# Performance work log

Measured on AMD Instinct MI355X. Metric: run time of the kernel, lower is better.

The kernel has to match this reference:

```python
import jax, jax.numpy as jnp
import numpy as np

HEADS = 8
NUM_LANDMARKS = 256
PINV_ITERS = 6
KERNEL = 33
PAD = KERNEL // 2


def moore_penrose_iter_pinv(x, iters=PINV_ITERS):
    abs_x = jnp.abs(x)
    col = abs_x.sum(axis=-1)
    row = abs_x.sum(axis=-2)
    z = jnp.swapaxes(x, -1, -2) / (jnp.max(col) * jnp.max(row))
    I = jnp.eye(x.shape[-1], dtype=x.dtype)
    for _ in range(iters):
        xz = x @ z
        z = 0.25 * z @ (13.0 * I - xz @ (15.0 * I - xz @ (7.0 * I - xz)))
    return z


def setup_inputs() -> dict:
    key = jax.random.key(0)
    k1, k2, k3, k4 = jax.random.split(key, 4)
    b, h, n, d = 2, HEADS, 8192, 64
    q = jax.random.normal(k1, (b, h, n, d), dtype=jnp.float32)
    k = jax.random.normal(k2, (b, h, n, d), dtype=jnp.float32)
    v = jax.random.normal(k3, (b, h, n, d), dtype=jnp.float32)
    conv_w = jax.random.normal(k4, (HEADS, 1, KERNEL, 1), dtype=jnp.float32) * 0.05
    return {"q": q, "k": k, "v": v, "conv_w": conv_w}


def reference(q, k, v, conv_w):
    b, h, n, d = q.shape
    m = NUM_LANDMARKS
    l = n // m  # n chosen divisible by m, so no padding branch

    # landmarks: mean over contiguous groups of size l
    q_land = q.reshape(b, h, m, l, d).sum(axis=-2) / l  # [b,h,m,d]
    k_land = k.reshape(b, h, m, l, d).sum(axis=-2) / l

    sim1 = jnp.einsum('bhid,bhjd->bhij', q, k_land)       # [b,h,n,m]
    sim2 = jnp.einsum('bhid,bhjd->bhij', q_land, k_land)  # [b,h,m,m]
    sim3 = jnp.einsum('bhid,bhjd->bhij', q_land, k)       # [b,h,m,n]

    attn1 = jax.nn.softmax(sim1, axis=-1)
    attn2 = jax.nn.softmax(sim2, axis=-1)
    attn3 = jax.nn.softmax(sim3, axis=-1)

    attn2_inv = moore_penrose_iter_pinv(attn2, PINV_ITERS)

    out = attn1 @ (attn2_inv @ (attn3 @ v))  # [b,h,n,d]

    # depthwise residual conv over sequence dim (Conv2d(h,h,(33,1),groups=h,bias=False) on v)
    res = jax.lax.conv_general_dilated(
        v, conv_w,
        window_strides=(1, 1),
        padding=((PAD, PAD), (0, 0)),
        dimension_numbers=('NCHW', 'OIHW', 'NCHW'),
        feature_group_count=HEADS,
    )
    return out + res
```

## Files before the change

kernel.cpp:

```cpp
#include <hip/hip_runtime.h>


#define N_SEQ 8192
#define NBH   16
#define MLAND 256
#define DHEAD 64
#define NSPLIT3 8

#define QT_STRIDE 132
#define KP_OFF    8448
#define WC_OFF    12800
#define FL_SMEM   17152

typedef __attribute__((ext_vector_type(8))) short bfrag;
typedef __attribute__((ext_vector_type(4))) float f32x4;

__device__ __forceinline__ void fma8(float (&o)[8], float p, const float4& a, const float4& b) {
    o[0] += p * a.x; o[1] += p * a.y; o[2] += p * a.z; o[3] += p * a.w;
    o[4] += p * b.x; o[5] += p * b.y; o[6] += p * b.z; o[7] += p * b.w;
}

__device__ __forceinline__ unsigned short f2bf(float f) {
    unsigned u = __float_as_uint(f);
    unsigned r = u + 0x7fffu + ((u >> 16) & 1u);
    return (unsigned short)(r >> 16);
}
__device__ __forceinline__ float bf2f(unsigned short h) {
    return __uint_as_float(((unsigned)h) << 16);
}

__device__ __forceinline__ void splitbf(float v, unsigned short& h, unsigned short& l) {
    unsigned bits = __float_as_uint(v);
    h = (unsigned short)(bits >> 16);
    float r = v - __uint_as_float(bits & 0xffff0000u);
    l = (unsigned short)(__float_as_uint(r) >> 16);
}

__device__ __forceinline__ void stage16(const float* __restrict__ src,
                                        unsigned short* dh, unsigned short* dl) {
    unsigned* ph = (unsigned*)dh;
    unsigned* pl = (unsigned*)dl;
    #pragma unroll
    for (int o = 0; o < 16; o += 4) {
        float4 a = *(const float4*)(src + o);
        float vv[4] = {a.x, a.y, a.z, a.w};
        unsigned short h[4], l[4];
        #pragma unroll
        for (int u = 0; u < 4; ++u) splitbf(vv[u], h[u], l[u]);
        ph[o / 2]     = (unsigned)h[0] | ((unsigned)h[1] << 16);
        ph[o / 2 + 1] = (unsigned)h[2] | ((unsigned)h[3] << 16);
        pl[o / 2]     = (unsigned)l[0] | ((unsigned)l[1] << 16);
        pl[o / 2 + 1] = (unsigned)l[2] | ((unsigned)l[3] << 16);
    }
}

__global__ __launch_bounds__(64) void k_landmarks(
    const float* __restrict__ q, const float* __restrict__ k,
    float* __restrict__ ql, float* __restrict__ kl)
{
    int mi = blockIdx.x & 255;
    int bh = blockIdx.x >> 8;
    const float* src = blockIdx.y ? k : q;
    float*       dst = blockIdx.y ? kl : ql;
    int t = threadIdx.x;
    const float* s = src + ((size_t)bh * N_SEQ + (size_t)mi * 32) * DHEAD;
    float acc = 0.f;
    #pragma unroll
    for (int j = 0; j < 32; ++j) acc += s[j * DHEAD + t];
    dst[((size_t)bh * MLAND + mi) * DHEAD + t] = acc * (1.f / 32.f);
}

__global__ __launch_bounds__(256) void k_sim2_softmax(
    const float* __restrict__ ql, const float* __restrict__ kl,
    float* __restrict__ attn2)
{
    int bh = blockIdx.x >> 8;
    int i  = blockIdx.x & 255;
    int t  = threadIdx.x;
    __shared__ float qrow[DHEAD];
    __shared__ float wred[8];
    if (t < DHEAD) qrow[t] = ql[((size_t)bh * MLAND + i) * DHEAD + t];
    __syncthreads();
    const float* krow = kl + ((size_t)bh * MLAND + t) * DHEAD;
    float s = 0.f;
    #pragma unroll
    for (int kk = 0; kk < DHEAD; kk += 4) {
        float4 k4 = *(const float4*)(krow + kk);
        s += qrow[kk] * k4.x + qrow[kk + 1] * k4.y + qrow[kk + 2] * k4.z + qrow[kk + 3] * k4.w;
    }
    float m = s;
    #pragma unroll
    for (int o = 32; o > 0; o >>= 1) m = fmaxf(m, __shfl_xor(m, o, 64));
    int wave = t >> 6, lane = t & 63;
    if (lane == 0) wred[wave] = m;
    __syncthreads();
    float bm = fmaxf(fmaxf(wred[0], wred[1]), fmaxf(wred[2], wred[3]));
    float e = __expf(s - bm);
    float sum = e;
    #pragma unroll
    for (int o = 32; o > 0; o >>= 1) sum += __shfl_xor(sum, o, 64);
    if (lane == 0) wred[4 + wave] = sum;
    __syncthreads();
    float bs = wred[4] + wred[5] + wred[6] + wred[7];
    attn2[((size_t)bh * MLAND + i) * MLAND + t] = e / bs;
}

__global__ __launch_bounds__(256) void k_scale_reduce(
    const float* __restrict__ x, float* __restrict__ scl)
{
    int bh = blockIdx.x, t = threadIdx.x;
    const float* xb = x + (size_t)bh * MLAND * MLAND;
    float colsum = 0.f, rowsum = 0.f;
    for (int i = 0; i < MLAND; ++i) colsum += xb[(size_t)i * MLAND + t];
    for (int j = 0; j < MLAND; ++j) rowsum += xb[(size_t)t * MLAND + j];
    __shared__ float red[256];
    red[t] = rowsum;
    __syncthreads();
    for (int o = 128; o > 0; o >>= 1) {
        if (t < o) red[t] = fmaxf(red[t], red[t + o]);
        __syncthreads();
    }
    if (t == 0) atomicMax((unsigned int*)&scl[0], __float_as_uint(red[0]));
    __syncthreads();
    red[t] = colsum;
    __syncthreads();
    for (int o = 128; o > 0; o >>= 1) {
        if (t < o) red[t] = fmaxf(red[t], red[t + o]);
        __syncthreads();
    }
    if (t == 0) atomicMax((unsigned int*)&scl[1], __float_as_uint(red[0]));
}

__global__ __launch_bounds__(256) void k_zinit(
    const float* __restrict__ x, float* __restrict__ z,
    const float* __restrict__ scl)
{
    __shared__ float tile[32][33];
    int bh = blockIdx.z;
    int i0 = blockIdx.y * 32, j0 = blockIdx.x * 32;
    int t = threadIdx.x;
    int lx = t & 31, ly = t >> 5;
    const float* xb = x + (size_t)bh * MLAND * MLAND;
    float*       zb = z + (size_t)bh * MLAND * MLAND;
    #pragma unroll
    for (int p = 0; p < 4; ++p)
        tile[ly + 8 * p][lx] = xb[(size_t)(i0 + ly + 8 * p) * MLAND + j0 + lx];
    __syncthreads();
    float inv = 1.0f / (scl[0] * scl[1]);
    #pragma unroll
    for (int p = 0; p < 4; ++p)
        zb[(size_t)(j0 + ly + 8 * p) * MLAND + i0 + lx] = tile[lx][ly + 8 * p] * inv;
}

__global__ __launch_bounds__(256) void k_bmm_mfma(
    const float* __restrict__ A, const float* __restrict__ B, float* __restrict__ C,
    int N, float diag, float bscale, float outscale)
{
    __shared__ unsigned short sm[4 * 64 * 72];
    unsigned short* Ah = sm;
    unsigned short* Al = sm + 64 * 72;
    unsigned short* Bh = sm + 2 * 64 * 72;
    unsigned short* Bl = sm + 3 * 64 * 72;

    int bh = blockIdx.z;
    const float* Ab = A + (size_t)bh * 65536;
    const float* Bb = B + (size_t)bh * 256 * N;
    float*       Cb = C + (size_t)bh * 256 * N;
    int m0 = blockIdx.y * 64, n0 = blockIdx.x * 64;
    int t = threadIdx.x;
    int wave = t >> 6, lane = t & 63;
    int l15 = lane & 15, quad = lane >> 4;

    f32x4 acc[4] = {};

    for (int kc = 0; kc < 256; kc += 64) {
        __syncthreads();
        {
            int m = t & 63, ks = (t >> 6) * 16;
            const float* src = Ab + (size_t)(m0 + m) * 256 + kc + ks;
            unsigned short h[16], l[16];
            #pragma unroll
            for (int o = 0; o < 16; o += 4) {
                float4 a = *(const float4*)(src + o);
                float vv[4] = {a.x, a.y, a.z, a.w};
                #pragma unroll
                for (int u = 0; u < 4; ++u) {
                    h[o + u] = f2bf(vv[u]);
                    l[o + u] = f2bf(vv[u] - bf2f(h[o + u]));
                }
            }
            unsigned* dh = (unsigned*)&Ah[m * 72 + ks];
            unsigned* dl = (unsigned*)&Al[m * 72 + ks];
            #pragma unroll
            for (int o = 0; o < 8; ++o) {
                dh[o] = (unsigned)h[2 * o] | ((unsigned)h[2 * o + 1] << 16);
                dl[o] = (unsigned)l[2 * o] | ((unsigned)l[2 * o + 1] << 16);
            }
        }
        {
            int kk = t & 63, ns = (t >> 6) * 16;
            int gk = kc + kk;
            const float* src = Bb + (size_t)gk * N + n0 + ns;
            #pragma unroll
            for (int o = 0; o < 16; o += 4) {
                float4 bv = *(const float4*)(src + o);
                float vv[4] = {bv.x, bv.y, bv.z, bv.w};
                #pragma unroll
                for (int u = 0; u < 4; ++u) {
                    float val = bscale * vv[u];
                    if (gk == n0 + ns + o + u) val += diag;
                    unsigned short hh = f2bf(val);
                    Bh[(ns + o + u) * 72 + kk] = hh;
                    Bl[(ns + o + u) * 72 + kk] = f2bf(val - bf2f(hh));
                }
            }
        }
        __syncthreads();

        #pragma unroll
        for (int k0 = 0; k0 < 64; k0 += 32) {
            int kf = k0 + quad * 8;
            int am = wave * 16 + l15;
            bfrag ah = *(const bfrag*)&Ah[am * 72 + kf];
            bfrag al = *(const bfrag*)&Al[am * 72 + kf];
            #pragma unroll
            for (int j = 0; j < 4; ++j) {
                int bn = j * 16 + l15;
                bfrag bhf = *(const bfrag*)&Bh[bn * 72 + kf];
                bfrag blf = *(const bfrag*)&Bl[bn * 72 + kf];
                acc[j] = __builtin_amdgcn_mfma_f32_16x16x32_bf16(al, bhf, acc[j], 0, 0, 0);
                acc[j] = __builtin_amdgcn_mfma_f32_16x16x32_bf16(ah, blf, acc[j], 0, 0, 0);
                acc[j] = __builtin_amdgcn_mfma_f32_16x16x32_bf16(ah, bhf, acc[j], 0, 0, 0);
            }
        }
    }

    #pragma unroll
    for (int j = 0; j < 4; ++j) {
        #pragma unroll
        for (int r = 0; r < 4; ++r) {
            int row = m0 + wave * 16 + quad * 4 + r;
            Cb[(size_t)row * N + n0 + j * 16 + l15] = acc[j][r] * outscale;
        }
    }
}

__global__ __launch_bounds__(256, 2) void k_attn3_partial(
    const float* __restrict__ ql, const float* __restrict__ k,
    const float* __restrict__ v, float* __restrict__ pO,
    float* __restrict__ pm, float* __restrict__ pl)
{
    __shared__ __align__(16) unsigned short sm3[36864];
    unsigned short* QH = sm3;
    unsigned short* QL = sm3 + 4608;
    unsigned short* KH = sm3 + 9216;
    unsigned short* KL = sm3 + 13824;
    unsigned short* VH = sm3 + 18432;
    unsigned short* VL = sm3 + 23040;
    unsigned short* PH = sm3 + 27648;
    unsigned short* PL = sm3 + 32256;

    int sp = blockIdx.x;
    int m0 = blockIdx.y * 64;
    int bh = blockIdx.z;
    int t = threadIdx.x;
    int wave = t >> 6, lane = t & 63;
    int l15 = lane & 15, quad = lane >> 4;

    {
        int row = t & 63, ds = (t >> 6) * 16;
        const float* src = ql + ((size_t)bh * MLAND + m0 + row) * DHEAD + ds;
        stage16(src, &QH[row * 72 + ds], &QL[row * 72 + ds]);
    }
    __syncthreads();

    bfrag aqh[2], aql[2];
    #pragma unroll
    for (int ks = 0; ks < 2; ++ks) {
        aqh[ks] = *(const bfrag*)&QH[(wave * 16 + l15) * 72 + ks * 32 + quad * 8];
        aql[ks] = *(const bfrag*)&QL[(wave * 16 + l15) * 72 + ks * 32 + quad * 8];
    }

    f32x4 O[4] = {};
    float M[4], L[4];
    #pragma unroll
    for (int r = 0; r < 4; ++r) { M[r] = -1e30f; L[r] = 0.f; }

    const float* kb = k + (size_t)bh * N_SEQ * DHEAD;
    const float* vb = v + (size_t)bh * N_SEQ * DHEAD;

    for (int cc = 0; cc < 16; ++cc) {
        int c0 = sp * 1024 + cc * 64;
        __syncthreads();
        {
            int key = t & 63, ds = (t >> 6) * 16;
            stage16(kb + (size_t)(c0 + key) * DHEAD + ds,
                    &KH[key * 72 + ds], &KL[key * 72 + ds]);
        }
        {
            int key = t & 63, dq = (t >> 6) * 16;
            const float* src = vb + (size_t)(c0 + key) * DHEAD + dq;
            #pragma unroll
            for (int o = 0; o < 16; o += 4) {
                float4 a = *(const float4*)(src + o);
                float vv[4] = {a.x, a.y, a.z, a.w};
                #pragma unroll
                for (int u = 0; u < 4; ++u) {
                    unsigned short h, l;
                    splitbf(vv[u], h, l);
                    VH[(dq + o + u) * 72 + key] = h;
                    VL[(dq + o + u) * 72 + key] = l;
                }
            }
        }
        __syncthreads();

        f32x4 S4[4] = {};
        __builtin_amdgcn_s_setprio(1);
        #pragma unroll
        for (int ks = 0; ks < 2; ++ks) {
            #pragma unroll
            for (int ni = 0; ni < 4; ++ni) {
                bfrag bkh = *(const bfrag*)&KH[(ni * 16 + l15) * 72 + ks * 32 + quad * 8];
                bfrag bkl = *(const bfrag*)&KL[(ni * 16 + l15) * 72 + ks * 32 + quad * 8];
                S4[ni] = __builtin_amdgcn_mfma_f32_16x16x32_bf16(aql[ks], bkh, S4[ni], 0, 0, 0);
                S4[ni] = __builtin_amdgcn_mfma_f32_16x16x32_bf16(aqh[ks], bkl, S4[ni], 0, 0, 0);
                S4[ni] = __builtin_amdgcn_mfma_f32_16x16x32_bf16(aqh[ks], bkh, S4[ni], 0, 0, 0);
            }
        }
        __builtin_amdgcn_s_setprio(0);

        #pragma unroll
        for (int r = 0; r < 4; ++r) {
            float mv = fmaxf(fmaxf(S4[0][r], S4[1][r]), fmaxf(S4[2][r], S4[3][r]));
            mv = fmaxf(mv, __shfl_xor(mv, 1, 16));
            mv = fmaxf(mv, __shfl_xor(mv, 2, 16));
            mv = fmaxf(mv, __shfl_xor(mv, 4, 16));
            mv = fmaxf(mv, __shfl_xor(mv, 8, 16));
            float nM = fmaxf(M[r], mv);
            float alpha = __expf(M[r] - nM);
            M[r] = nM;
            float rs = 0.f;
            #pragma unroll
            for (int ni = 0; ni < 4; ++ni) {
                float p = __expf(S4[ni][r] - nM);
                S4[ni][r] = p;
                rs += p;
            }
            rs += __shfl_xor(rs, 1, 16);
            rs += __shfl_xor(rs, 2, 16);
            rs += __shfl_xor(rs, 4, 16);
            rs += __shfl_xor(rs, 8, 16);
            L[r] = L[r] * alpha + rs;
            #pragma unroll
            for (int ni = 0; ni < 4; ++ni) O[ni][r] *= alpha;
        }

        #pragma unroll
        for (int ni = 0; ni < 4; ++ni) {
            #pragma unroll
            for (int r = 0; r < 4; ++r) {
                int row = wave * 16 + quad * 4 + r;
                int col = ni * 16 + l15;
                unsigned short h, l;
                splitbf(S4[ni][r], h, l);
                PH[row * 72 + col] = h;
                PL[row * 72 + col] = l;
            }
        }

        __builtin_amdgcn_s_setprio(1);
        #pragma unroll
        for (int ks = 0; ks < 2; ++ks) {
            bfrag aph = *(const bfrag*)&PH[(wave * 16 + l15) * 72 + ks * 32 + quad * 8];
            bfrag apl = *(const bfrag*)&PL[(wave * 16 + l15) * 72 + ks * 32 + quad * 8];
            #pragma unroll
            for (int ni = 0; ni < 4; ++ni) {
                bfrag bvh = *(const bfrag*)&VH[(ni * 16 + l15) * 72 + ks * 32 + quad * 8];
                bfrag bvl = *(const bfrag*)&VL[(ni * 16 + l15) * 72 + ks * 32 + quad * 8];
                O[ni] = __builtin_amdgcn_mfma_f32_16x16x32_bf16(apl, bvh, O[ni], 0, 0, 0);
                O[ni] = __builtin_amdgcn_mfma_f32_16x16x32_bf16(aph, bvl, O[ni], 0, 0, 0);
                O[ni] = __builtin_amdgcn_mfma_f32_16x16x32_bf16(aph, bvh, O[ni], 0, 0, 0);
            }
        }
        __builtin_amdgcn_s_setprio(0);
    }

    int base = (bh * NSPLIT3 + sp) * MLAND + m0;
    #pragma unroll
    for (int r = 0; r < 4; ++r) {
        int row = wave * 16 + quad * 4 + r;
        if (l15 == 0) { pm[base + row] = M[r]; pl[base + row] = L[r]; }
        #pragma unroll
        for (int ni = 0; ni < 4; ++ni)
            pO[(size_t)(base + row) * DHEAD + ni * 16 + l15] = O[ni][r];
    }
}

__global__ __launch_bounds__(64) void k_attn3_combine(
    const float* __restrict__ pO, const float* __restrict__ pm,
    const float* __restrict__ pl, float* __restrict__ kv)
{
    int bh = blockIdx.x >> 8;
    int m  = blockIdx.x & 255;
    int d  = threadIdx.x;
    float M = -1e30f;
    #pragma unroll
    for (int s = 0; s < NSPLIT3; ++s) M = fmaxf(M, pm[(bh * NSPLIT3 + s) * MLAND + m]);
    float L = 0.f, O = 0.f;
    #pragma unroll
    for (int s = 0; s < NSPLIT3; ++s) {
        int base = (bh * NSPLIT3 + s) * MLAND + m;
        float w = __expf(pm[base] - M);
        L += pl[base] * w;
        O += w * pO[(size_t)base * DHEAD + d];
    }
    kv[((size_t)bh * MLAND + m) * DHEAD + d] = O / L;
}

__global__ __launch_bounds__(256, 2) void k_attn1_out(
    const float* __restrict__ q, const float* __restrict__ kl,
    const float* __restrict__ W, const float* __restrict__ v,
    const float* __restrict__ cw, float* __restrict__ out)
{
    __shared__ __align__(16) float smem[FL_SMEM];
    __shared__ float wgt[33];
    int bh = blockIdx.y;
    int r0 = blockIdx.x * 128;
    int t = threadIdx.x;
    int wave = t >> 6, lane = t & 63;
    int ly = lane >> 3, lx = lane & 7;
    int rb = wave * 32 + ly * 4;

    if (t < 33) wgt[t] = cw[(bh & 7) * 33 + t];
    {
        int m = t >> 1, k0 = (t & 1) * 32;
        const float* src = q + ((size_t)bh * N_SEQ + r0 + m) * DHEAD + k0;
        #pragma unroll
        for (int kk = 0; kk < 32; kk += 4) {
            float4 a = *(const float4*)(src + kk);
            smem[(k0 + kk + 0) * QT_STRIDE + m] = a.x;
            smem[(k0 + kk + 1) * QT_STRIDE + m] = a.y;
            smem[(k0 + kk + 2) * QT_STRIDE + m] = a.z;
            smem[(k0 + kk + 3) * QT_STRIDE + m] = a.w;
        }
    }

    float S[4][8], O[4][8] = {};
    float M[4], L[4];
    #pragma unroll
    for (int i = 0; i < 4; ++i) { M[i] = -1e30f; L[i] = 0.f; }

    for (int mc = 0; mc < 4; ++mc) {
        __syncthreads();
        {
            int j = t & 63, kq = t >> 6;
            const float* src = kl + ((size_t)bh * MLAND + mc * 64 + j) * DHEAD + kq * 16;
            #pragma unroll
            for (int o = 0; o < 16; o += 4) {
                float4 a = *(const float4*)(src + o);
                smem[KP_OFF + (kq * 16 + o + 0) * 68 + j] = a.x;
                smem[KP_OFF + (kq * 16 + o + 1) * 68 + j] = a.y;
                smem[KP_OFF + (kq * 16 + o + 2) * 68 + j] = a.z;
                smem[KP_OFF + (kq * 16 + o + 3) * 68 + j] = a.w;
            }
        }
        {
            int j = t & 63, dq = t >> 6;
            const float* src = W + ((size_t)bh * MLAND + mc * 64 + j) * DHEAD + dq * 16;
            #pragma unroll
            for (int o = 0; o < 16; o += 4)
                *(float4*)&smem[WC_OFF + j * 68 + dq * 16 + o] = *(const float4*)(src + o);
        }
        __syncthreads();

        #pragma unroll
        for (int i = 0; i < 4; ++i)
            #pragma unroll
            for (int j = 0; j < 8; ++j) S[i][j] = 0.f;
        #pragma unroll 4
        for (int kk = 0; kk < DHEAD; ++kk) {
            float4 a4 = *(const float4*)&smem[kk * QT_STRIDE + rb];
            float4 b0 = *(const float4*)&smem[KP_OFF + kk * 68 + lx * 8];
            float4 b1 = *(const float4*)&smem[KP_OFF + kk * 68 + lx * 8 + 4];
            float av[4] = {a4.x, a4.y, a4.z, a4.w};
            #pragma unroll
            for (int i = 0; i < 4; ++i) fma8(S[i], av[i], b0, b1);
        }

        #pragma unroll
        for (int i = 0; i < 4; ++i) {
            float mv = S[i][0];
            #pragma unroll
            for (int j = 1; j < 8; ++j) mv = fmaxf(mv, S[i][j]);
            mv = fmaxf(mv, __shfl_xor(mv, 4, 8));
            mv = fmaxf(mv, __shfl_xor(mv, 2, 8));
            mv = fmaxf(mv, __shfl_xor(mv, 1, 8));
            float nM = fmaxf(M[i], mv);
            float alpha = __expf(M[i] - nM);
            M[i] = nM;
            float rs = 0.f;
            #pragma unroll
            for (int j = 0; j < 8; ++j) { S[i][j] = __expf(S[i][j] - nM); rs += S[i][j]; }
            rs += __shfl_xor(rs, 4, 8);
            rs += __shfl_xor(rs, 2, 8);
            rs += __shfl_xor(rs, 1, 8);
            L[i] = L[i] * alpha + rs;
            #pragma unroll
            for (int j = 0; j < 8; ++j) O[i][j] *= alpha;
        }

        #pragma unroll 2
        for (int lsrc = 0; lsrc < 8; ++lsrc) {
            #pragma unroll
            for (int jq = 0; jq < 8; ++jq) {
                int j = lsrc * 8 + jq;
                float4 v0 = *(const float4*)&smem[WC_OFF + j * 68 + lx * 8];
                float4 v1 = *(const float4*)&smem[WC_OFF + j * 68 + lx * 8 + 4];
                #pragma unroll
                for (int i = 0; i < 4; ++i) {
                    float p = __shfl(S[i][jq], lsrc, 8);
                    fma8(O[i], p, v0, v1);
                }
            }
        }
    }

    float inv[4];
    #pragma unroll
    for (int i = 0; i < 4; ++i) inv[i] = 1.0f / L[i];

    __syncthreads();
    for (int rr = t; rr < 160; rr += 256) {
        int gr = r0 - 16 + rr;
        bool ok = (gr >= 0) && (gr < N_SEQ);
        const float* src = v + ((size_t)bh * N_SEQ + gr) * DHEAD;
        #pragma unroll
        for (int c = 0; c < 64; c += 4) {
            float4 val = ok ? *(const float4*)(src + c) : make_float4(0.f, 0.f, 0.f, 0.f);
            *(float4*)&smem[rr * 68 + c] = val;
        }
    }
    __syncthreads();

    float res[4][8] = {};
    #pragma unroll
    for (int w = 0; w < 36; ++w) {
        float4 va = *(const float4*)&smem[(rb + w) * 68 + lx * 8];
        float4 vb4 = *(const float4*)&smem[(rb + w) * 68 + lx * 8 + 4];
        #pragma unroll
        for (int i = 0; i < 4; ++i) {
            if (w - i >= 0 && w - i <= 32) {
                float wv = wgt[w - i];
                fma8(res[i], wv, va, vb4);
            }
        }
    }

    #pragma unroll
    for (int i = 0; i < 4; ++i) {
        float* dst = out + ((size_t)bh * N_SEQ + r0 + rb + i) * DHEAD + lx * 8;
        *(float4*)dst = make_float4(O[i][0] * inv[i] + res[i][0], O[i][1] * inv[i] + res[i][1],
                                    O[i][2] * inv[i] + res[i][2], O[i][3] * inv[i] + res[i][3]);
        *(float4*)(dst + 4) = make_float4(O[i][4] * inv[i] + res[i][4], O[i][5] * inv[i] + res[i][5],
                                          O[i][6] * inv[i] + res[i][6], O[i][7] * inv[i] + res[i][7]);
    }
}

extern "C" void kernel_launch(void* const* d_in, const int* in_sizes, int n_in,
                              void* d_out, int out_size, void* d_ws, size_t ws_size,
                              hipStream_t stream)
{
    (void)in_sizes; (void)n_in; (void)out_size; (void)ws_size;
    const float* q  = (const float*)d_in[0];
    const float* k  = (const float*)d_in[1];
    const float* v  = (const float*)d_in[2];
    const float* cw = (const float*)d_in[3];
    float* out = (float*)d_out;
    float* ws  = (float*)d_ws;

    const size_t LM = (size_t)NBH * MLAND * DHEAD;
    const size_t MM = (size_t)NBH * MLAND * MLAND;
    float* ql  = ws;
    float* kl  = ql  + LM;
    float* x   = kl  + LM;
    float* z   = x   + MM;
    float* z2  = z   + MM;
    float* xz  = z2  + MM;
    float* t2  = xz  + MM;
    float* t3  = t2  + MM;
    float* kv  = t3  + MM;
    float* W   = kv  + LM;
    float* scl = W   + LM;
    float* pm  = scl + 16;
    float* pl  = pm + (size_t)NBH * 16 * MLAND;

    float* pO = z2;

    hipMemsetAsync(scl, 0, 32, stream);

    k_landmarks<<<dim3(NBH * MLAND, 2), 64, 0, stream>>>(q, k, ql, kl);
    k_sim2_softmax<<<NBH * MLAND, 256, 0, stream>>>(ql, kl, x);
    k_scale_reduce<<<NBH, 256, 0, stream>>>(x, scl);
    k_zinit<<<dim3(8, 8, NBH), 256, 0, stream>>>(x, z, scl);

    k_attn3_partial<<<dim3(NSPLIT3, 4, NBH), 256, 0, stream>>>(ql, k, v, pO, pm, pl);
    k_attn3_combine<<<NBH * MLAND, 64, 0, stream>>>(pO, pm, pl, kv);

    float* zc = z;
    float* zn = z2;
    for (int it = 0; it < 6; ++it) {
        k_bmm_mfma<<<dim3(4, 4, NBH), 256, 0, stream>>>(x,  zc, xz, 256,  0.f,  1.f, 1.f);
        k_bmm_mfma<<<dim3(4, 4, NBH), 256, 0, stream>>>(xz, xz, t2, 256,  7.f, -1.f, 1.f);
        k_bmm_mfma<<<dim3(4, 4, NBH), 256, 0, stream>>>(xz, t2, t3, 256, 15.f, -1.f, 1.f);
        k_bmm_mfma<<<dim3(4, 4, NBH), 256, 0, stream>>>(zc, t3, zn, 256, 13.f, -1.f, 0.25f);
        float* tt = zc; zc = zn; zn = tt;
    }
    k_bmm_mfma<<<dim3(1, 4, NBH), 256, 0, stream>>>(zc, kv, W, 64, 0.f, 1.f, 1.f);

    k_attn1_out<<<dim3(64, NBH), 256, 0, stream>>>(q, kl, W, v, cw, out);
}
```

Measured before the change: 707.3 us.

## Move attn1 output to split-fp16 MFMA and split conv residual into separate kernel

Replaces the scalar-FMA attn1 softmax and output kernel with one using fp16 MFMA. Each operand is split into high and low fp16 parts and three MFMAs are issued to keep near-fp32 accuracy, with W pre-scaled by 1/64 to avoid fp16 overflow. The depthwise conv residual moves into a separate kernel that reads the attention output back and adds to it. This trades an extra launch and an extra read/write of the output for much higher matrix throughput and smaller tiles of 64 rows.

```diff
diff --git a/kernel.cpp b/kernel.cpp
--- a/kernel.cpp
+++ b/kernel.cpp
@@ -7,12 +7,8 @@
 #define DHEAD 64
 #define NSPLIT3 8
 
-#define QT_STRIDE 132
-#define KP_OFF    8448
-#define WC_OFF    12800
-#define FL_SMEM   17152
-
 typedef __attribute__((ext_vector_type(8))) short bfrag;
+typedef __attribute__((ext_vector_type(8))) _Float16 hfrag;
 typedef __attribute__((ext_vector_type(4))) float f32x4;
 
 __device__ __forceinline__ void fma8(float (&o)[8], float p, const float4& a, const float4& b) {
@@ -36,6 +32,13 @@
     l = (unsigned short)(__float_as_uint(r) >> 16);
 }
 
+__device__ __forceinline__ void splith(float v, unsigned short& h, unsigned short& l) {
+    _Float16 hf = (_Float16)v;
+    _Float16 lf = (_Float16)(v - (float)hf);
+    h = __builtin_bit_cast(unsigned short, hf);
+    l = __builtin_bit_cast(unsigned short, lf);
+}
+
 __device__ __forceinline__ void stage16(const float* __restrict__ src,
                                         unsigned short* dh, unsigned short* dl) {
     unsigned* ph = (unsigned*)dh;
@@ -47,6 +50,24 @@
         unsigned short h[4], l[4];
         #pragma unroll
         for (int u = 0; u < 4; ++u) splitbf(vv[u], h[u], l[u]);
+        ph[o / 2]     = (unsigned)h[0] | ((unsigned)h[1] << 16);
+        ph[o / 2 + 1] = (unsigned)h[2] | ((unsigned)h[3] << 16);
+        pl[o / 2]     = (unsigned)l[0] | ((unsigned)l[1] << 16);
+        pl[o / 2 + 1] = (unsigned)l[2] | ((unsigned)l[3] << 16);
+    }
+}
+
+__device__ __forceinline__ void stageh16(const float* __restrict__ src,
+                                         unsigned short* dh, unsigned short* dl) {
+    unsigned* ph = (unsigned*)dh;
+    unsigned* pl = (unsigned*)dl;
+    #pragma unroll
+    for (int o = 0; o < 16; o += 4) {
+        float4 a = *(const float4*)(src + o);
+        float vv[4] = {a.x, a.y, a.z, a.w};
+        unsigned short h[4], l[4];
+        #pragma unroll
+        for (int u = 0; u < 4; ++u) splith(vv[u], h[u], l[u]);
         ph[o / 2]     = (unsigned)h[0] | ((unsigned)h[1] << 16);
         ph[o / 2 + 1] = (unsigned)h[2] | ((unsigned)h[3] << 16);
         pl[o / 2]     = (unsigned)l[0] | ((unsigned)l[1] << 16);
@@ -418,12 +439,160 @@
     kv[((size_t)bh * MLAND + m) * DHEAD + d] = O / L;
 }
 
-__global__ __launch_bounds__(256, 2) void k_attn1_out(
+__global__ __launch_bounds__(256, 2) void k_attn1_mfma(
     const float* __restrict__ q, const float* __restrict__ kl,
-    const float* __restrict__ W, const float* __restrict__ v,
-    const float* __restrict__ cw, float* __restrict__ out)
-{
-    __shared__ __align__(16) float smem[FL_SMEM];
+    const float* __restrict__ W, float* __restrict__ out)
+{
+    __shared__ __align__(16) unsigned short sm1[36864];
+    unsigned short* QH = sm1;
+    unsigned short* QL = sm1 + 4608;
+    unsigned short* KH = sm1 + 9216;
+    unsigned short* KL = sm1 + 13824;
+    unsigned short* WH = sm1 + 18432;
+    unsigned short* WL = sm1 + 23040;
+    unsigned short* PH = sm1 + 27648;
+    unsigned short* PL = sm1 + 32256;
+
+    int bh = blockIdx.y;
+    int r0 = blockIdx.x * 64;
+    int t = threadIdx.x;
+    int wave = t >> 6, lane = t & 63;
+    int l15 = lane & 15, quad = lane >> 4;
+
+    {
+        int row = t & 63, ds = (t >> 6) * 16;
+        const float* src = q + ((size_t)bh * N_SEQ + r0 + row) * DHEAD + ds;
+        stageh16(src, &QH[row * 72 + ds], &QL[row * 72 + ds]);
+    }
+    __syncthreads();
+
+    hfrag aqh[2], aql[2];
+    #pragma unroll
+    for (int ks = 0; ks < 2; ++ks) {
+        aqh[ks] = *(const hfrag*)&QH[(wave * 16 + l15) * 72 + ks * 32 + quad * 8];
+        aql[ks] = *(const hfrag*)&QL[(wave * 16 + l15) * 72 + ks * 32 + quad * 8];
+    }
+
+    f32x4 O4[4] = {};
+    float M[4], L[4];
+    #pragma unroll
+    for (int r = 0; r < 4; ++r) { M[r] = -1e30f; L[r] = 0.f; }
+
+    for (int mc = 0; mc < 4; ++mc) {
+        __syncthreads();
+        {
+            int key = t & 63, ds = (t >> 6) * 16;
+            stageh16(kl + ((size_t)bh * MLAND + mc * 64 + key) * DHEAD + ds,
+                     &KH[key * 72 + ds], &KL[key * 72 + ds]);
+        }
+        {
+            int key = t & 63, dq = (t >> 6) * 16;
+            const float* src = W + ((size_t)bh * MLAND + mc * 64 + key) * DHEAD + dq;
+            #pragma unroll
+            for (int o = 0; o < 16; o += 4) {
+                float4 a = *(const float4*)(src + o);
+                float vv[4] = {a.x * 0.015625f, a.y * 0.015625f,
+                               a.z * 0.015625f, a.w * 0.015625f};
+                #pragma unroll
+                for (int u = 0; u < 4; ++u) {
+                    unsigned short h, l;
+                    splith(vv[u], h, l);
+                    WH[(dq + o + u) * 72 + key] = h;
+                    WL[(dq + o + u) * 72 + key] = l;
+                }
+            }
+        }
+        __syncthreads();
+
+        f32x4 S4[4] = {};
+        __builtin_amdgcn_s_setprio(1);
+        #pragma unroll
+        for (int ks = 0; ks < 2; ++ks) {
+            #pragma unroll
+            for (int ni = 0; ni < 4; ++ni) {
+                hfrag bkh = *(const hfrag*)&KH[(ni * 16 + l15) * 72 + ks * 32 + quad * 8];
+                hfrag bkl = *(const hfrag*)&KL[(ni * 16 + l15) * 72 + ks * 32 + quad * 8];
+                S4[ni] = __builtin_amdgcn_mfma_f32_16x16x32_f16(aql[ks], bkh, S4[ni], 0, 0, 0);
+                S4[ni] = __builtin_amdgcn_mfma_f32_16x16x32_f16(aqh[ks], bkl, S4[ni], 0, 0, 0);
+                S4[ni] = __builtin_amdgcn_mfma_f32_16x16x32_f16(aqh[ks], bkh, S4[ni], 0, 0, 0);
+            }
+        }
+        __builtin_amdgcn_s_setprio(0);
+
+        #pragma unroll
+        for (int r = 0; r < 4; ++r) {
+            float mv = fmaxf(fmaxf(S4[0][r], S4[1][r]), fmaxf(S4[2][r], S4[3][r]));
+            mv = fmaxf(mv, __shfl_xor(mv, 1, 16));
+            mv = fmaxf(mv, __shfl_xor(mv, 2, 16));
+            mv = fmaxf(mv, __shfl_xor(mv, 4, 16));
+            mv = fmaxf(mv, __shfl_xor(mv, 8, 16));
+            float nM = fmaxf(M[r], mv);
+            float alpha = __expf(M[r] - nM);
+            M[r] = nM;
+            float rs = 0.f;
+            #pragma unroll
+            for (int ni = 0; ni < 4; ++ni) {
+                float p = __expf(S4[ni][r] - nM);
+                S4[ni][r] = p;
+                rs += p;
+            }
+            rs += __shfl_xor(rs, 1, 16);
+            rs += __shfl_xor(rs, 2, 16);
+            rs += __shfl_xor(rs, 4, 16);
+            rs += __shfl_xor(rs, 8, 16);
+            L[r] = L[r] * alpha + rs;
+            #pragma unroll
+            for (int ni = 0; ni < 4; ++ni) O4[ni][r] *= alpha;
+        }
+
+        #pragma unroll
+        for (int ni = 0; ni < 4; ++ni) {
+            #pragma unroll
+            for (int r = 0; r < 4; ++r) {
+                int row = wave * 16 + quad * 4 + r;
+                int col = ni * 16 + l15;
+                unsigned short h, l;
+                splith(S4[ni][r], h, l);
+                PH[row * 72 + col] = h;
+                PL[row * 72 + col] = l;
+            }
+        }
+
+        __builtin_amdgcn_s_setprio(1);
+        #pragma unroll
+        for (int ks = 0; ks < 2; ++ks) {
+            hfrag aph = *(const hfrag*)&PH[(wave * 16 + l15) * 72 + ks * 32 + quad * 8];
+            hfrag apl = *(const hfrag*)&PL[(wave * 16 + l15) * 72 + ks * 32 + quad * 8];
+            #pragma unroll
+            for (int ni = 0; ni < 4; ++ni) {
+                hfrag bwh = *(const hfrag*)&WH[(ni * 16 + l15) * 72 + ks * 32 + quad * 8];
+                hfrag bwl = *(const hfrag*)&WL[(ni * 16 + l15) * 72 + ks * 32 + quad * 8];
+                O4[ni] = __builtin_amdgcn_mfma_f32_16x16x32_f16(apl, bwh, O4[ni], 0, 0, 0);
+                O4[ni] = __builtin_amdgcn_mfma_f32_16x16x32_f16(aph, bwl, O4[ni], 0, 0, 0);
+                O4[ni] = __builtin_amdgcn_mfma_f32_16x16x32_f16(aph, bwh, O4[ni], 0, 0, 0);
+            }
+        }
+        __builtin_amdgcn_s_setprio(0);
+    }
+
+    float inv[4];
+    #pragma unroll
+    for (int r = 0; r < 4; ++r) inv[r] = 64.0f / L[r];
+    #pragma unroll
+    for (int r = 0; r < 4; ++r) {
+        int row = wave * 16 + quad * 4 + r;
+        float* dst = out + ((size_t)bh * N_SEQ + r0 + row) * DHEAD;
+        #pragma unroll
+        for (int ni = 0; ni < 4; ++ni)
+            dst[ni * 16 + l15] = O4[ni][r] * inv[r];
+    }
+}
+
+__global__ __launch_bounds__(256) void k_conv_add(
+    const float* __restrict__ v, const float* __restrict__ cw,
+    float* __restrict__ out)
+{
+    __shared__ __align__(16) float smem[160 * 68];
     __shared__ float wgt[33];
     int bh = blockIdx.y;
     int r0 = blockIdx.x * 128;
@@ -433,104 +602,7 @@
     int rb = wave * 32 + ly * 4;
 
     if (t < 33) wgt[t] = cw[(bh & 7) * 33 + t];
-    {
-        int m = t >> 1, k0 = (t & 1) * 32;
-        const float* src = q + ((size_t)bh * N_SEQ + r0 + m) * DHEAD + k0;
-        #pragma unroll
-        for (int kk = 0; kk < 32; kk += 4) {
-            float4 a = *(const float4*)(src + kk);
-            smem[(k0 + kk + 0) * QT_STRIDE + m] = a.x;
-            smem[(k0 + kk + 1) * QT_STRIDE + m] = a.y;
-            smem[(k0 + kk + 2) * QT_STRIDE + m] = a.z;
-            smem[(k0 + kk + 3) * QT_STRIDE + m] = a.w;
-        }
-    }
-
-    float S[4][8], O[4][8] = {};
-    float M[4], L[4];
-    #pragma unroll
-    for (int i = 0; i < 4; ++i) { M[i] = -1e30f; L[i] = 0.f; }
-
-    for (int mc = 0; mc < 4; ++mc) {
-        __syncthreads();
-        {
-            int j = t & 63, kq = t >> 6;
-            const float* src = kl + ((size_t)bh * MLAND + mc * 64 + j) * DHEAD + kq * 16;
-            #pragma unroll
-            for (int o = 0; o < 16; o += 4) {
-                float4 a = *(const float4*)(src + o);
-                smem[KP_OFF + (kq * 16 + o + 0) * 68 + j] = a.x;
-                smem[KP_OFF + (kq * 16 + o + 1) * 68 + j] = a.y;
-                smem[KP_OFF + (kq * 16 + o + 2) * 68 + j] = a.z;
-                smem[KP_OFF + (kq * 16 + o + 3) * 68 + j] = a.w;
-            }
-        }
-        {
-            int j = t & 63, dq = t >> 6;
-            const float* src = W + ((size_t)bh * MLAND + mc * 64 + j) * DHEAD + dq * 16;
-            #pragma unroll
-            for (int o = 0; o < 16; o += 4)
-                *(float4*)&smem[WC_OFF + j * 68 + dq * 16 + o] = *(const float4*)(src + o);
-        }
-        __syncthreads();
-
-        #pragma unroll
-        for (int i = 0; i < 4; ++i)
-            #pragma unroll
-            for (int j = 0; j < 8; ++j) S[i][j] = 0.f;
-        #pragma unroll 4
-        for (int kk = 0; kk < DHEAD; ++kk) {
-            float4 a4 = *(const float4*)&smem[kk * QT_STRIDE + rb];
-            float4 b0 = *(const float4*)&smem[KP_OFF + kk * 68 + lx * 8];
-            float4 b1 = *(const float4*)&smem[KP_OFF + kk * 68 + lx * 8 + 4];
-            float av[4] = {a4.x, a4.y, a4.z, a4.w};
-            #pragma unroll
-            for (int i = 0; i < 4; ++i) fma8(S[i], av[i], b0, b1);
-        }
-
-        #pragma unroll
-        for (int i = 0; i < 4; ++i) {
-            float mv = S[i][0];
-            #pragma unroll
-            for (int j = 1; j < 8; ++j) mv = fmaxf(mv, S[i][j]);
-            mv = fmaxf(mv, __shfl_xor(mv, 4, 8));
-            mv = fmaxf(mv, __shfl_xor(mv, 2, 8));
-            mv = fmaxf(mv, __shfl_xor(mv, 1, 8));
-            float nM = fmaxf(M[i], mv);
-            float alpha = __expf(M[i] - nM);
-            M[i] = nM;
-            float rs = 0.f;
-            #pragma unroll
-            for (int j = 0; j < 8; ++j) { S[i][j] = __expf(S[i][j] - nM); rs += S[i][j]; }
-            rs += __shfl_xor(rs, 4, 8);
-            rs += __shfl_xor(rs, 2, 8);
-            rs += __shfl_xor(rs, 1, 8);
-            L[i] = L[i] * alpha + rs;
-            #pragma unroll
-            for (int j = 0; j < 8; ++j) O[i][j] *= alpha;
-        }
-
-        #pragma unroll 2
-        for (int lsrc = 0; lsrc < 8; ++lsrc) {
-            #pragma unroll
-            for (int jq = 0; jq < 8; ++jq) {
-                int j = lsrc * 8 + jq;
-                float4 v0 = *(const float4*)&smem[WC_OFF + j * 68 + lx * 8];
-                float4 v1 = *(const float4*)&smem[WC_OFF + j * 68 + lx * 8 + 4];
-                #pragma unroll
-                for (int i = 0; i < 4; ++i) {
-                    float p = __shfl(S[i][jq], lsrc, 8);
-                    fma8(O[i], p, v0, v1);
-                }
-            }
-        }
-    }
-
-    float inv[4];
-    #pragma unroll
-    for (int i = 0; i < 4; ++i) inv[i] = 1.0f / L[i];
-
-    __syncthreads();
+
     for (int rr = t; rr < 160; rr += 256) {
         int gr = r0 - 16 + rr;
         bool ok = (gr >= 0) && (gr < N_SEQ);
@@ -546,7 +618,7 @@
     float res[4][8] = {};
     #pragma unroll
     for (int w = 0; w < 36; ++w) {
-        float4 va = *(const float4*)&smem[(rb + w) * 68 + lx * 8];
+        float4 va  = *(const float4*)&smem[(rb + w) * 68 + lx * 8];
         float4 vb4 = *(const float4*)&smem[(rb + w) * 68 + lx * 8 + 4];
         #pragma unroll
         for (int i = 0; i < 4; ++i) {
@@ -560,10 +632,12 @@
     #pragma unroll
     for (int i = 0; i < 4; ++i) {
         float* dst = out + ((size_t)bh * N_SEQ + r0 + rb + i) * DHEAD + lx * 8;
-        *(float4*)dst = make_float4(O[i][0] * inv[i] + res[i][0], O[i][1] * inv[i] + res[i][1],
-                                    O[i][2] * inv[i] + res[i][2], O[i][3] * inv[i] + res[i][3]);
-        *(float4*)(dst + 4) = make_float4(O[i][4] * inv[i] + res[i][4], O[i][5] * inv[i] + res[i][5],
-                                          O[i][6] * inv[i] + res[i][6], O[i][7] * inv[i] + res[i][7]);
+        float4 o0 = *(const float4*)dst;
+        float4 o1 = *(const float4*)(dst + 4);
+        *(float4*)dst = make_float4(o0.x + res[i][0], o0.y + res[i][1],
+                                    o0.z + res[i][2], o0.w + res[i][3]);
+        *(float4*)(dst + 4) = make_float4(o1.x + res[i][4], o1.y + res[i][5],
+                                          o1.z + res[i][6], o1.w + res[i][7]);
     }
 }
 
@@ -618,5 +692,6 @@
     }
     k_bmm_mfma<<<dim3(1, 4, NBH), 256, 0, stream>>>(zc, kv, W, 64, 0.f, 1.f, 1.f);
 
-    k_attn1_out<<<dim3(64, NBH), 256, 0, stream>>>(q, kl, W, v, cw, out);
-}
+    k_attn1_mfma<<<dim3(128, NBH), 256, 0, stream>>>(q, kl, W, out);
+    k_conv_add<<<dim3(64, NBH), 256, 0, stream>>>(v, cw, out);
+}
```

Measured after the change: 645.2 us. 8.8% less time.
